# Optimization experiments

Measured on AMD Instinct MI355X. Metric: run time of the kernel, lower is better.

Reference implementation:

```python
import jax, jax.numpy as jnp
import numpy as np

B, CIN, H, W = 256, 1280, 7, 7
A, NCLS, HID, NGT = 9, 20, 128, 40
OUT_DIM = 5 * A + NCLS  # 65


def setup_inputs() -> dict:
    key = jax.random.key(0)
    ks = jax.random.split(key, 8)
    features = jax.random.normal(ks[0], (B, CIN, H, W), jnp.float32)
    # grid: (x, y) centers of each feature cell, in feature-map coordinates
    grid = jax.random.uniform(ks[1], (B, H, W, 2), jnp.float32) * 7.0
    # GT boxes (x1, y1, x2, y2, class), padded count NGT per image
    xy1 = jax.random.uniform(ks[2], (B, NGT, 2), jnp.float32) * 5.0
    wh = jax.random.uniform(ks[3], (B, NGT, 2), jnp.float32) * 2.0 + 0.5
    cls = jax.random.randint(ks[4], (B, NGT, 1), 0, NCLS).astype(jnp.float32)
    bboxes = jnp.concatenate([xy1, xy1 + wh, cls], axis=-1)
    # anchor shapes (w, h) as in SingleStageDetector.__init__
    anc = jnp.array([[1.0, 1], [2, 2], [3, 3], [4, 4], [5, 5],
                     [2, 3], [3, 2], [3, 5], [5, 3]], jnp.float32)
    W1 = jax.random.normal(ks[5], (HID, CIN), jnp.float32) * 0.02
    b1 = jnp.zeros((HID,), jnp.float32)
    W2 = jax.random.normal(ks[6], (OUT_DIM, HID), jnp.float32) * 0.02
    b2 = jnp.zeros((OUT_DIM,), jnp.float32)
    return dict(features=features, grid=grid, bboxes=bboxes, anc=anc,
                W1=W1, b1=b1, W2=W2, b2=b2)


def reference(features, grid, bboxes, anc, W1, b1, W2, b2):
    Bx = features.shape[0]
    # --- PredictionNetwork (inference mode; dropout is identity at eval) ---
    h = jnp.einsum('bchw,oc->bohw', features, W1) + b1[None, :, None, None]
    h = jax.nn.leaky_relu(h, negative_slope=0.01)
    out = jnp.einsum('bchw,oc->bohw', h, W2) + b2[None, :, None, None]
    conf_scores = jax.nn.sigmoid(out[:, 4 * A:5 * A])          # (B, A, H, W)
    offsets = out[:, :4 * A].reshape(Bx, A, 4, H, W)
    offsets = jnp.concatenate(
        [jax.nn.sigmoid(offsets[:, :, :2]) - 0.5, offsets[:, :, 2:]], axis=2)
    class_scores = out[:, 5 * A:]                               # (B, C, H, W)
    # --- GenerateAnchor: (B, A, H, W, 4) as (x_tl, y_tl, x_br, y_br) ---
    ctr = grid[:, None]                    # (B, 1, H, W, 2)
    half = anc[None, :, None, None, :] / 2  # (1, A, 1, 1, 2)
    anchors = jnp.concatenate([ctr - half, ctr + half], axis=-1)
    # --- IoU: (B, A*H*W, N) ---
    P = anchors.reshape(Bx, -1, 4)          # (B, AHW, 4)
    gt = bboxes[..., :4]                    # (B, N, 4)
    tl = jnp.maximum(P[:, :, None, :2], gt[:, None, :, :2])
    br = jnp.minimum(P[:, :, None, 2:], gt[:, None, :, 2:])
    inter = jnp.prod(jnp.clip(br - tl, 0.0), axis=-1)  # (B, AHW, N)
    # torch code zeroes intersections for proposals with any coord <= 0
    legal = (jnp.min(P, axis=-1) > 0)[..., None]
    inter = inter * legal
    p_area = ((P[:, :, 2] - P[:, :, 0]) * (P[:, :, 3] - P[:, :, 1]))[:, :, None]
    g_area = ((gt[:, :, 2] - gt[:, :, 0]) * (gt[:, :, 3] - gt[:, :, 1]))[:, None, :]
    iou_mat = inter / (g_area + p_area - inter)
    return (conf_scores, offsets, class_scores, iou_mat)
```

## Files before the change

### kernel.cpp

```cpp
#include <hip/hip_runtime.h>


#define CIN_  1280
#define HW_   49
#define HID_  128
#define OUTD_ 65
#define NGT_  40
#define NP_   441

#define CONF_OFF 0
#define OFFS_OFF 112896
#define CLS_OFF  564480
#define IOU_OFF  815360

#define WS_W1F_U32 81920u
#define WS_W2F_U32 5120u

typedef __bf16 bf16x8 __attribute__((ext_vector_type(8)));
typedef float  f32x4  __attribute__((ext_vector_type(4)));

__device__ __forceinline__ unsigned pack2bf(float lo, float hi) {
    unsigned a = __float_as_uint(lo);
    unsigned b = __float_as_uint(hi);
    a = (a + 0x7FFFu + ((a >> 16) & 1u)) >> 16;
    b = (b + 0x7FFFu + ((b >> 16) & 1u)) >> 16;
    return a | (b << 16);
}
__device__ __forceinline__ float sigmoidf_(float v) { return 1.f / (1.f + __expf(-v)); }

__device__ __forceinline__ bf16x8 ld_frag(const unsigned* p) {
    union { uint4 u; bf16x8 v; } x;
    x.u = *(const uint4*)p;
    return x.v;
}
__device__ __forceinline__ bf16x8 as_bf(uint4 u) {
    union { uint4 u; bf16x8 v; } x; x.u = u; return x.v;
}

__global__ __launch_bounds__(256) void prep_w(
    const float* __restrict__ W1, const float* __restrict__ W2,
    unsigned* __restrict__ ws)
{
    int X = blockIdx.x * 256 + threadIdx.x;
    if (X < (int)WS_W1F_U32) {
        int sub = X & 3, lane = (X >> 2) & 63, f = X >> 8;
        int mt = f & 7, K32 = f >> 3;
        int o = mt * 16 + (lane & 15);
        int c = K32 * 32 + (lane >> 4) * 8 + sub * 2;
        float2 v = *(const float2*)(W1 + o * CIN_ + c);
        ws[X] = pack2bf(v.x, v.y);
    } else {
        int Y = X - (int)WS_W1F_U32;
        int sub = Y & 3, lane = (Y >> 2) & 63, f = Y >> 8;
        int mt2 = f % 5, ks2 = f / 5;
        int o2 = mt2 * 16 + (lane & 15);
        int c = ks2 * 32 + (lane >> 4) * 8 + sub * 2;
        unsigned val = 0;
        if (o2 < OUTD_) {
            float2 v = *(const float2*)(W2 + o2 * HID_ + c);
            val = pack2bf(v.x, v.y);
        }
        ws[WS_W1F_U32 + Y] = val;
    }
}

__global__ __launch_bounds__(512, 4) void fused_main(
    const float* __restrict__ F,
    const float* __restrict__ grd,
    const float* __restrict__ bbox,
    const float* __restrict__ anc,
    const unsigned* __restrict__ wsW,
    const float* __restrict__ B1,
    const float* __restrict__ B2,
    float* __restrict__ out)
{
    __shared__ __align__(16) unsigned lds[2 * 32 * 128];
    unsigned* smHT = lds;

    const int tid  = threadIdx.x;
    const int b    = blockIdx.x >> 1;
    const int half = blockIdx.x & 1;
    const int lane = tid & 63;
    const int w    = tid >> 6;
    const int quad = lane >> 4;
    const int m16  = lane & 15;
    const int hw0  = half * 32;

    const float* Fb = F + b * (CIN_ * HW_);

    const int srow = tid & 31;
    const int shw  = hw0 + srow;
    const bool sok = shw < HW_;
    const int cb0  = (tid >> 5) * 2;
    const float* Fs = Fb + shw;

    float fl[16];
    #define STAGE_ISSUE(c)                                                   \
        {                                                                    \
            _Pragma("unroll")                                                \
            for (int u = 0; u < 2; ++u) {                                    \
                _Pragma("unroll")                                            \
                for (int j = 0; j < 8; ++j) {                                \
                    int ch = (c) * 256 + (cb0 + u) * 8 + j;                  \
                    fl[u * 8 + j] = sok ? Fs[ch * HW_] : 0.f;                \
                }                                                            \
            }                                                                \
        }
    #define STAGE_WRITE(c)                                                   \
        {                                                                    \
            unsigned* dstb = lds + (((c) & 1) << 12) + srow * 128;           \
            _Pragma("unroll")                                                \
            for (int u = 0; u < 2; ++u) {                                    \
                int cb = cb0 + u;                                            \
                uint4 q;                                                     \
                q.x = pack2bf(fl[u * 8 + 0], fl[u * 8 + 1]);                 \
                q.y = pack2bf(fl[u * 8 + 2], fl[u * 8 + 3]);                 \
                q.z = pack2bf(fl[u * 8 + 4], fl[u * 8 + 5]);                 \
                q.w = pack2bf(fl[u * 8 + 6], fl[u * 8 + 7]);                 \
                *(uint4*)(dstb + ((cb ^ (srow & 7)) << 2)) = q;              \
            }                                                                \
        }

    STAGE_ISSUE(0);
    const uint4* Ap = (const uint4*)wsW + w * 64 + lane;
    uint4 a0 = Ap[0];
    uint4 a1 = Ap[512];
    STAGE_WRITE(0);
    __syncthreads();

    const unsigned* r0base = lds + m16 * 128;
    const unsigned* r1base = lds + (16 + m16) * 128;
    const int swz = (m16 & 7);

    f32x4 acc0 = (f32x4)(0.f), acc1 = (f32x4)(0.f);
    int kglob = 0;
    #pragma unroll
    for (int c = 0; c < 5; ++c) {
        if (c < 4) STAGE_ISSUE(c + 1);
        const int boff = (c & 1) << 12;
        #pragma unroll
        for (int kk = 0; kk < 8; ++kk) {
            int kp = kglob + 2; if (kp > 39) kp = 39;
            uint4 an = Ap[kp * 512];
            int off = (((kk << 2) + quad) ^ swz) << 2;
            bf16x8 A = as_bf(a0);
            acc0 = __builtin_amdgcn_mfma_f32_16x16x32_bf16(A, ld_frag(r0base + boff + off), acc0, 0, 0, 0);
            acc1 = __builtin_amdgcn_mfma_f32_16x16x32_bf16(A, ld_frag(r1base + boff + off), acc1, 0, 0, 0);
            a0 = a1; a1 = an; ++kglob;
        }
        if (c < 4) STAGE_WRITE(c + 1);
        __syncthreads();
    }

    const int m2a = w % 5, nt2a = w / 5;
    const uint4* A2p = (const uint4*)(wsW + WS_W1F_U32) + m2a * 64 + lane;
    uint4 a20 = A2p[0], a21 = A2p[320], a22 = A2p[640], a23 = A2p[960];

    #pragma unroll
    for (int nt = 0; nt < 2; ++nt) {
        f32x4 ac = nt ? acc1 : acc0;
        int r0 = nt * 16 + m16;
        #pragma unroll
        for (int rp = 0; rp < 2; ++rp) {
            int o0 = w * 16 + quad * 4 + 2 * rp;
            float v0 = ac[2 * rp]     + B1[o0];
            float v1 = ac[2 * rp + 1] + B1[o0 + 1];
            v0 = v0 > 0.f ? v0 : 0.01f * v0;
            v1 = v1 > 0.f ? v1 : 0.01f * v1;
            smHT[r0 * 68 + (o0 >> 1)] = pack2bf(v0, v1);
        }
    }
    __syncthreads();

    {
        f32x4 c2 = (f32x4)(0.f);
        const unsigned* Bb = smHT + (nt2a * 16 + m16) * 68 + quad * 4;
        c2 = __builtin_amdgcn_mfma_f32_16x16x32_bf16(as_bf(a20), ld_frag(Bb +  0), c2, 0, 0, 0);
        c2 = __builtin_amdgcn_mfma_f32_16x16x32_bf16(as_bf(a21), ld_frag(Bb + 16), c2, 0, 0, 0);
        c2 = __builtin_amdgcn_mfma_f32_16x16x32_bf16(as_bf(a22), ld_frag(Bb + 32), c2, 0, 0, 0);
        c2 = __builtin_amdgcn_mfma_f32_16x16x32_bf16(as_bf(a23), ld_frag(Bb + 48), c2, 0, 0, 0);
        int hw = hw0 + nt2a * 16 + m16;
        if (hw < HW_) {
            #pragma unroll
            for (int r = 0; r < 4; ++r) {
                int o2 = m2a * 16 + quad * 4 + r;
                if (o2 >= OUTD_) continue;
                float aa = c2[r] + B2[o2];
                unsigned dst; float val;
                if (o2 < 36) {
                    int an9 = o2 >> 2, kk = o2 & 3;
                    val = (kk < 2) ? (sigmoidf_(aa) - 0.5f) : aa;
                    dst = OFFS_OFF + b * 1764 + an9 * 196 + kk * 49 + hw;
                } else if (o2 < 45) {
                    val = sigmoidf_(aa);
                    dst = CONF_OFF + b * 441 + (o2 - 36) * 49 + hw;
                } else {
                    val = aa;
                    dst = CLS_OFF + b * 980 + (o2 - 45) * 49 + hw;
                }
                out[dst] = val;
            }
        }
    }
    if (w < 2) {
        const int m2b = 3 + w;
        const uint4* A3p = (const uint4*)(wsW + WS_W1F_U32) + m2b * 64 + lane;
        uint4 b20 = A3p[0], b21 = A3p[320], b22 = A3p[640], b23 = A3p[960];
        f32x4 c2 = (f32x4)(0.f);
        const unsigned* Bb = smHT + (16 + m16) * 68 + quad * 4;
        c2 = __builtin_amdgcn_mfma_f32_16x16x32_bf16(as_bf(b20), ld_frag(Bb +  0), c2, 0, 0, 0);
        c2 = __builtin_amdgcn_mfma_f32_16x16x32_bf16(as_bf(b21), ld_frag(Bb + 16), c2, 0, 0, 0);
        c2 = __builtin_amdgcn_mfma_f32_16x16x32_bf16(as_bf(b22), ld_frag(Bb + 32), c2, 0, 0, 0);
        c2 = __builtin_amdgcn_mfma_f32_16x16x32_bf16(as_bf(b23), ld_frag(Bb + 48), c2, 0, 0, 0);
        int hw = hw0 + 16 + m16;
        if (hw < HW_) {
            #pragma unroll
            for (int r = 0; r < 4; ++r) {
                int o2 = m2b * 16 + quad * 4 + r;
                if (o2 >= OUTD_) continue;
                float aa = c2[r] + B2[o2];
                unsigned dst; float val;
                if (o2 < 36) {
                    int an9 = o2 >> 2, kk = o2 & 3;
                    val = (kk < 2) ? (sigmoidf_(aa) - 0.5f) : aa;
                    dst = OFFS_OFF + b * 1764 + an9 * 196 + kk * 49 + hw;
                } else if (o2 < 45) {
                    val = sigmoidf_(aa);
                    dst = CONF_OFF + b * 441 + (o2 - 36) * 49 + hw;
                } else {
                    val = aa;
                    dst = CLS_OFF + b * 980 + (o2 - 45) * 49 + hw;
                }
                out[dst] = val;
            }
        }
    }

    {
        int gl = (lane < NGT_) ? lane : 0;
        const float* gb = bbox + b * 200 + gl * 5;
        float gx1 = gb[0], gy1 = gb[1], gx2 = gb[2], gy2 = gb[3];
        float gA = (gx2 - gx1) * (gy2 - gy1);
        const int pstart = half ? 221 : 0;
        const int pend   = half ? NP_ : 221;
        #pragma unroll 4
        for (int p = pstart + w; p < pend; p += 8) {
            int a9 = p / 49, r = p - a9 * 49;
            float2 ct = *(const float2*)(grd + b * 98 + 2 * r);
            float hx = anc[2 * a9] * 0.5f,  hy = anc[2 * a9 + 1] * 0.5f;
            float px1 = ct.x - hx, py1 = ct.y - hy, px2 = ct.x + hx, py2 = ct.y + hy;
            float pA = (px2 - px1) * (py2 - py1);
            float legal = (fminf(fminf(px1, py1), fminf(px2, py2)) > 0.f) ? 1.f : 0.f;
            float tlx = fmaxf(px1, gx1), tly = fmaxf(py1, gy1);
            float brx = fminf(px2, gx2), bry = fminf(py2, gy2);
            float dx = fmaxf(brx - tlx, 0.f), dy = fmaxf(bry - tly, 0.f);
            float inter = dx * dy * legal;
            float iou = inter / (gA + pA - inter);
            if (lane < NGT_)
                out[IOU_OFF + b * (NP_ * NGT_) + p * 40 + lane] = iou;
        }
    }
}

extern "C" void kernel_launch(void* const* d_in, const int* in_sizes, int n_in,
                              void* d_out, int out_size, void* d_ws, size_t ws_size,
                              hipStream_t stream) {
    const float* F  = (const float*)d_in[0];
    const float* G  = (const float*)d_in[1];
    const float* BB = (const float*)d_in[2];
    const float* AN = (const float*)d_in[3];
    const float* W1 = (const float*)d_in[4];
    const float* B1 = (const float*)d_in[5];
    const float* W2 = (const float*)d_in[6];
    const float* B2 = (const float*)d_in[7];
    float* out = (float*)d_out;
    unsigned* wsu = (unsigned*)d_ws;

    prep_w<<<340, 256, 0, stream>>>(W1, W2, wsu);
    fused_main<<<512, 512, 0, stream>>>(F, G, BB, AN, wsu, B1, B2, out);
}
```

Baseline: 135.6 us.

## Deepen feature prefetch to two stages and overlap IoU with loads

Feature staging now keeps two chunks of global loads in flight using double-buffered registers, instead of one. The IoU computation moves to before the first LDS write, so its work and stores hide the latency of the first prefetched loads. Padding rows are zero-filled once up front rather than masked per load. bf16 packing now uses the builtin conversion and the IoU divide uses a fast approximate divide. Together these raise register pressure, and the fast divide may change IoU precision slightly.

```diff
diff --git a/kernel.cpp b/kernel.cpp
--- a/kernel.cpp
+++ b/kernel.cpp
@@ -20,11 +20,9 @@
 typedef float  f32x4  __attribute__((ext_vector_type(4)));
 
 __device__ __forceinline__ unsigned pack2bf(float lo, float hi) {
-    unsigned a = __float_as_uint(lo);
-    unsigned b = __float_as_uint(hi);
-    a = (a + 0x7FFFu + ((a >> 16) & 1u)) >> 16;
-    b = (b + 0x7FFFu + ((b >> 16) & 1u)) >> 16;
-    return a | (b << 16);
+    unsigned short a = __builtin_bit_cast(unsigned short, (__bf16)lo);
+    unsigned short b = __builtin_bit_cast(unsigned short, (__bf16)hi);
+    return (unsigned)a | ((unsigned)b << 16);
 }
 __device__ __forceinline__ float sigmoidf_(float v) { return 1.f / (1.f + __expf(-v)); }
 
@@ -94,37 +92,73 @@
     const int cb0  = (tid >> 5) * 2;
     const float* Fs = Fb + shw;
 
-    float fl[16];
+    float fl[2][16];
     #define STAGE_ISSUE(c)                                                   \
-        {                                                                    \
+        if (sok) {                                                           \
             _Pragma("unroll")                                                \
             for (int u = 0; u < 2; ++u) {                                    \
                 _Pragma("unroll")                                            \
                 for (int j = 0; j < 8; ++j) {                                \
                     int ch = (c) * 256 + (cb0 + u) * 8 + j;                  \
-                    fl[u * 8 + j] = sok ? Fs[ch * HW_] : 0.f;                \
+                    fl[(c) & 1][u * 8 + j] = Fs[ch * HW_];                   \
                 }                                                            \
             }                                                                \
         }
     #define STAGE_WRITE(c)                                                   \
-        {                                                                    \
+        if (sok) {                                                           \
             unsigned* dstb = lds + (((c) & 1) << 12) + srow * 128;           \
             _Pragma("unroll")                                                \
             for (int u = 0; u < 2; ++u) {                                    \
                 int cb = cb0 + u;                                            \
                 uint4 q;                                                     \
-                q.x = pack2bf(fl[u * 8 + 0], fl[u * 8 + 1]);                 \
-                q.y = pack2bf(fl[u * 8 + 2], fl[u * 8 + 3]);                 \
-                q.z = pack2bf(fl[u * 8 + 4], fl[u * 8 + 5]);                 \
-                q.w = pack2bf(fl[u * 8 + 6], fl[u * 8 + 7]);                 \
+                q.x = pack2bf(fl[(c) & 1][u * 8 + 0], fl[(c) & 1][u * 8 + 1]); \
+                q.y = pack2bf(fl[(c) & 1][u * 8 + 2], fl[(c) & 1][u * 8 + 3]); \
+                q.z = pack2bf(fl[(c) & 1][u * 8 + 4], fl[(c) & 1][u * 8 + 5]); \
+                q.w = pack2bf(fl[(c) & 1][u * 8 + 6], fl[(c) & 1][u * 8 + 7]); \
                 *(uint4*)(dstb + ((cb ^ (srow & 7)) << 2)) = q;              \
             }                                                                \
         }
 
+    if (!sok) {
+        uint4 z = {0u, 0u, 0u, 0u};
+        #pragma unroll
+        for (int bf = 0; bf < 2; ++bf) {
+            unsigned* dstb = lds + (bf << 12) + srow * 128;
+            *(uint4*)(dstb + (((cb0    ) ^ (srow & 7)) << 2)) = z;
+            *(uint4*)(dstb + (((cb0 + 1) ^ (srow & 7)) << 2)) = z;
+        }
+    }
     STAGE_ISSUE(0);
     const uint4* Ap = (const uint4*)wsW + w * 64 + lane;
     uint4 a0 = Ap[0];
     uint4 a1 = Ap[512];
+    STAGE_ISSUE(1);
+
+    {
+        int gl = (lane < NGT_) ? lane : 0;
+        const float* gb = bbox + b * 200 + gl * 5;
+        float gx1 = gb[0], gy1 = gb[1], gx2 = gb[2], gy2 = gb[3];
+        float gA = (gx2 - gx1) * (gy2 - gy1);
+        const int pstart = half ? 221 : 0;
+        const int pend   = half ? NP_ : 221;
+        #pragma unroll 4
+        for (int p = pstart + w; p < pend; p += 8) {
+            int a9 = p / 49, r = p - a9 * 49;
+            float2 ct = *(const float2*)(grd + b * 98 + 2 * r);
+            float hx = anc[2 * a9] * 0.5f,  hy = anc[2 * a9 + 1] * 0.5f;
+            float px1 = ct.x - hx, py1 = ct.y - hy, px2 = ct.x + hx, py2 = ct.y + hy;
+            float pA = (px2 - px1) * (py2 - py1);
+            float legal = (fminf(fminf(px1, py1), fminf(px2, py2)) > 0.f) ? 1.f : 0.f;
+            float tlx = fmaxf(px1, gx1), tly = fmaxf(py1, gy1);
+            float brx = fminf(px2, gx2), bry = fminf(py2, gy2);
+            float dx = fmaxf(brx - tlx, 0.f), dy = fmaxf(bry - tly, 0.f);
+            float inter = dx * dy * legal;
+            float iou = __fdividef(inter, gA + pA - inter);
+            if (lane < NGT_)
+                out[IOU_OFF + b * (NP_ * NGT_) + p * 40 + lane] = iou;
+        }
+    }
+
     STAGE_WRITE(0);
     __syncthreads();
 
@@ -136,7 +170,7 @@
     int kglob = 0;
     #pragma unroll
     for (int c = 0; c < 5; ++c) {
-        if (c < 4) STAGE_ISSUE(c + 1);
+        if (c < 3) STAGE_ISSUE(c + 2);
         const int boff = (c & 1) << 12;
         #pragma unroll
         for (int kk = 0; kk < 8; ++kk) {
@@ -235,31 +269,6 @@
             }
         }
     }
-
-    {
-        int gl = (lane < NGT_) ? lane : 0;
-        const float* gb = bbox + b * 200 + gl * 5;
-        float gx1 = gb[0], gy1 = gb[1], gx2 = gb[2], gy2 = gb[3];
-        float gA = (gx2 - gx1) * (gy2 - gy1);
-        const int pstart = half ? 221 : 0;
-        const int pend   = half ? NP_ : 221;
-        #pragma unroll 4
-        for (int p = pstart + w; p < pend; p += 8) {
-            int a9 = p / 49, r = p - a9 * 49;
-            float2 ct = *(const float2*)(grd + b * 98 + 2 * r);
-            float hx = anc[2 * a9] * 0.5f,  hy = anc[2 * a9 + 1] * 0.5f;
-            float px1 = ct.x - hx, py1 = ct.y - hy, px2 = ct.x + hx, py2 = ct.y + hy;
-            float pA = (px2 - px1) * (py2 - py1);
-            float legal = (fminf(fminf(px1, py1), fminf(px2, py2)) > 0.f) ? 1.f : 0.f;
-            float tlx = fmaxf(px1, gx1), tly = fmaxf(py1, gy1);
-            float brx = fminf(px2, gx2), bry = fminf(py2, gy2);
-            float dx = fmaxf(brx - tlx, 0.f), dy = fmaxf(bry - tly, 0.f);
-            float inter = dx * dy * legal;
-            float iou = inter / (gA + pA - inter);
-            if (lane < NGT_)
-                out[IOU_OFF + b * (NP_ * NGT_) + p * 40 + lane] = iou;
-        }
-    }
 }
 
 extern "C" void kernel_launch(void* const* d_in, const int* in_sizes, int n_in,
```

Measured after the change: 131.9 us. 2.8% less time.
